# Performance work log

Hardware: AMD Instinct MI355X
Metric: run time of the kernel (lower is better)

The kernel has to match this reference:

```python
import jax, jax.numpy as jnp
import numpy as np

H = 16
D = 1024
Dh = D // H


def setup_inputs() -> dict:
    key = jax.random.key(0)
    ks = jax.random.split(key, 11)
    B, S = 2, 2048
    s = 1.0 / np.sqrt(D)
    inp = {
        'q': jax.random.normal(ks[0], (B, S, D), jnp.float32),
        'k': jax.random.normal(ks[1], (B, S, D), jnp.float32),
        'v': jax.random.normal(ks[2], (B, S, D), jnp.float32),
        'Wq': jax.random.normal(ks[3], (D, D), jnp.float32) * s,
        'bq': jnp.zeros((D,), jnp.float32),
        'Wk': jax.random.normal(ks[4], (D, D), jnp.float32) * s,
        'bk': jnp.zeros((D,), jnp.float32),
        'Wv': jax.random.normal(ks[5], (D, D), jnp.float32) * s,
        'bv': jnp.zeros((D,), jnp.float32),
        'Wo': jax.random.normal(ks[6], (D, D), jnp.float32) * s,
        'bo': jnp.zeros((D,), jnp.float32),
    }
    return inp


def reference(q, k, v, Wq, bq, Wk, bk, Wv, bv, Wo, bo):
    B, S, _ = q.shape
    # Linear projections (torch Linear: x @ W.T + b)
    qh = (q @ Wq.T + bq).reshape(B, S, H, Dh).transpose(0, 2, 1, 3)  # [B,H,S,Dh]
    kh = (k @ Wk.T + bk).reshape(B, S, H, Dh).transpose(0, 2, 1, 3)
    vh = (v @ Wv.T + bv).reshape(B, S, H, Dh).transpose(0, 2, 1, 3)
    # Scaled dot-product attention (mask=None, dropout=identity at eval)
    scores = jnp.einsum('bhqd,bhkd->bhqk', qh, kh) / jnp.sqrt(jnp.float32(Dh))
    a = jax.nn.softmax(scores, axis=-1)  # [B,H,S,S]
    o = jnp.einsum('bhqk,bhkd->bhqd', a, vh)
    o = o.transpose(0, 2, 1, 3).reshape(B, S, D)
    o = o @ Wo.T + bo
    return (o, a)
```

## Files before the change

kernel.cpp:

```cpp
#include <hip/hip_runtime.h>

typedef unsigned short u16;
typedef __bf16 bf16x8 __attribute__((ext_vector_type(8)));
typedef float f32x4 __attribute__((ext_vector_type(4)));

#define MFMA_BF16(a,b,c) __builtin_amdgcn_mfma_f32_16x16x32_bf16((a),(b),(c),0,0,0)

#define Bc 2
#define Sc 2048
#define Dc 1024
#define Hc 16
#define Dh 64
#define Mrows (Bc*Sc)

#define OFF_QB   0u
#define OFF_KB   4194304u
#define OFF_VB   8388608u
#define OFF_WQB  12582912u
#define OFF_WKB  13631488u
#define OFF_WVB  14680064u
#define OFF_WOB  15728640u
#define OFF_QP   16777216u
#define OFF_KP   20971520u
#define OFF_VP   25165824u
#define OFF_VT   29360128u
#define OFF_OH   33554432u

__device__ __forceinline__ u16 f32_to_bf16(float f) {
  unsigned u = __builtin_bit_cast(unsigned, f);
  u += 0x7FFFu + ((u >> 16) & 1u);
  return (u16)(u >> 16);
}
__device__ __forceinline__ float bf16_to_f32(u16 x) {
  return __builtin_bit_cast(float, ((unsigned)x) << 16);
}

__device__ __forceinline__ void gload16(const u16* g, u16* l) {
  __builtin_amdgcn_global_load_lds(
      (__attribute__((address_space(1))) void*)(g),
      (__attribute__((address_space(3))) void*)(l),
      16, 0, 0);
}

__global__ __launch_bounds__(256) void cvt_all(
    const float* __restrict__ q, const float* __restrict__ k, const float* __restrict__ v,
    const float* __restrict__ wq, const float* __restrict__ wk,
    const float* __restrict__ wv, const float* __restrict__ wo,
    u16* __restrict__ ws)
{
  int y = blockIdx.y;
  const float* src; u16* dst; int n;
  if (y < 3) {
    src = (y == 0) ? q : (y == 1) ? k : v;
    dst = ws + (unsigned)y * 4194304u;
    n = 4194304;
  } else {
    src = (y == 3) ? wq : (y == 4) ? wk : (y == 5) ? wv : wo;
    dst = ws + OFF_WQB + (unsigned)(y - 3) * 1048576u;
    n = 1048576;
  }
  int i = (blockIdx.x * 256 + threadIdx.x) * 8;
  if (i >= n) return;
  float4 f0 = *(const float4*)(src + i);
  float4 f1 = *(const float4*)(src + i + 4);
  u16 o[8];
  o[0] = f32_to_bf16(f0.x); o[1] = f32_to_bf16(f0.y);
  o[2] = f32_to_bf16(f0.z); o[3] = f32_to_bf16(f0.w);
  o[4] = f32_to_bf16(f1.x); o[5] = f32_to_bf16(f1.y);
  o[6] = f32_to_bf16(f1.z); o[7] = f32_to_bf16(f1.w);
  *(uint4*)(dst + i) = *(uint4*)o;
}

__device__ __forceinline__ void gemm128_body(
    const u16* __restrict__ X, const u16* __restrict__ W, const float* __restrict__ bias,
    u16* __restrict__ out_bf, float* __restrict__ out_f,
    u16* As, u16* Bs, int m0, int n0)
{
  int tid = threadIdx.x;
  int lane = tid & 63, w = tid >> 6;
  int wr = w >> 1, wc = w & 1;
  int qd = lane >> 4, ln = lane & 15;

  f32x4 acc[4][4];
#pragma unroll
  for (int i = 0; i < 4; i++)
#pragma unroll
    for (int j = 0; j < 4; j++) acc[i][j] = f32x4{0.f, 0.f, 0.f, 0.f};

  int srow = w * 16 + (lane >> 2);
  int scol = (lane & 3) * 8;
  const u16* Xa = X + (size_t)(m0 + srow) * 1024 + scol;
  const u16* Xb = Xa + (size_t)64 * 1024;
  const u16* Wa = W + (size_t)(n0 + srow) * 1024 + scol;
  const u16* Wb = Wa + (size_t)64 * 1024;
  u16* asA0 = As + (w * 16) * 32;
  u16* asA1 = As + (w * 16 + 64) * 32;
  u16* asB0 = Bs + (w * 16) * 32;
  u16* asB1 = Bs + (w * 16 + 64) * 32;

  for (int k0 = 0; k0 < 1024; k0 += 32) {
    __syncthreads();
    gload16(Xa + k0, asA0);
    gload16(Xb + k0, asA1);
    gload16(Wa + k0, asB0);
    gload16(Wb + k0, asB1);
    __syncthreads();
    bf16x8 af[4], bfr[4];
#pragma unroll
    for (int i = 0; i < 4; i++)
      af[i] = *(const bf16x8*)&As[(wr * 64 + i * 16 + ln) * 32 + qd * 8];
#pragma unroll
    for (int j = 0; j < 4; j++)
      bfr[j] = *(const bf16x8*)&Bs[(wc * 64 + j * 16 + ln) * 32 + qd * 8];
#pragma unroll
    for (int i = 0; i < 4; i++)
#pragma unroll
      for (int j = 0; j < 4; j++)
        acc[i][j] = MFMA_BF16(af[i], bfr[j], acc[i][j]);
  }

#pragma unroll
  for (int i = 0; i < 4; i++) {
#pragma unroll
    for (int j = 0; j < 4; j++) {
      int col = n0 + wc * 64 + j * 16 + ln;
      float bv = bias[col];
#pragma unroll
      for (int r = 0; r < 4; r++) {
        int row = m0 + wr * 64 + i * 16 + qd * 4 + r;
        float val = acc[i][j][r] + bv;
        if (out_bf) out_bf[(size_t)row * 1024 + col] = f32_to_bf16(val);
        else        out_f[(size_t)row * 1024 + col]  = val;
      }
    }
  }
}

__global__ __launch_bounds__(256) void qkv_gemm(
    const u16* __restrict__ xq, const u16* __restrict__ xk, const u16* __restrict__ xv,
    const u16* __restrict__ wq, const u16* __restrict__ wk, const u16* __restrict__ wv,
    const float* __restrict__ bq, const float* __restrict__ bk, const float* __restrict__ bv,
    u16* __restrict__ Qp, u16* __restrict__ Kp, u16* __restrict__ Vp)
{
  __shared__ __attribute__((aligned(16))) u16 As[128 * 32];
  __shared__ __attribute__((aligned(16))) u16 Bs[128 * 32];
  const u16 *X, *W; const float* bias; u16* out;
  int z = blockIdx.z;
  if (z == 0)      { X = xq; W = wq; bias = bq; out = Qp; }
  else if (z == 1) { X = xk; W = wk; bias = bk; out = Kp; }
  else             { X = xv; W = wv; bias = bv; out = Vp; }
  gemm128_body(X, W, bias, out, nullptr, As, Bs, blockIdx.y * 128, blockIdx.x * 128);
}

__global__ __launch_bounds__(256) void out_gemm(
    const u16* __restrict__ Oh, const u16* __restrict__ Wo, const float* __restrict__ bo,
    float* __restrict__ out)
{
  __shared__ __attribute__((aligned(16))) u16 As[128 * 32];
  __shared__ __attribute__((aligned(16))) u16 Bs[128 * 32];
  gemm128_body(Oh, Wo, bo, nullptr, out, As, Bs, blockIdx.y * 128, blockIdx.x * 128);
}

__global__ __launch_bounds__(256) void transpose_v(const u16* __restrict__ Vp, u16* __restrict__ Vt)
{
  __shared__ __attribute__((aligned(16))) u16 T[64 * 72];
  int tid = threadIdx.x;
  int st = blockIdx.x;
  int bh = blockIdx.y;
  int b = bh >> 4, h = bh & 15;
  int r0 = tid >> 3, c0 = (tid & 7) * 8;
  const u16* src = Vp + (size_t)(b * Sc + st * 64) * Dc + h * 64;
  *(uint4*)&T[r0 * 72 + c0]        = *(const uint4*)&src[(size_t)r0 * Dc + c0];
  *(uint4*)&T[(r0 + 32) * 72 + c0] = *(const uint4*)&src[(size_t)(r0 + 32) * Dc + c0];
  __syncthreads();
  u16* dst = Vt + (size_t)bh * 64 * Sc + st * 64;
  u16 tmp[8];
#pragma unroll
  for (int i = 0; i < 8; i++) tmp[i] = T[(c0 + i) * 72 + r0];
  *(uint4*)&dst[(size_t)r0 * Sc + c0] = *(uint4*)tmp;
#pragma unroll
  for (int i = 0; i < 8; i++) tmp[i] = T[(c0 + i) * 72 + r0 + 32];
  *(uint4*)&dst[(size_t)(r0 + 32) * Sc + c0] = *(uint4*)tmp;
}

#define BUFW (64 * 72)

__global__ __launch_bounds__(256) void attn_kernel(
    const u16* __restrict__ Qp, const u16* __restrict__ Kp, const u16* __restrict__ Vt,
    float* __restrict__ a_out, u16* __restrict__ Oh)
{
  __shared__ __attribute__((aligned(16))) u16 pool[5 * BUFW];
  __shared__ float Lb[4][64];
  u16* buf0 = pool;
  u16* buf1 = pool + BUFW;
  u16* buf2 = pool + 2 * BUFW;
  u16* buf3 = pool + 3 * BUFW;
  u16* Ps   = pool + 4 * BUFW;

  int tid = threadIdx.x;
  int lane = tid & 63, w = tid >> 6;
  int qd = lane >> 4, ln = lane & 15;
  int qb = blockIdx.x;
  int bh = blockIdx.y;
  int b = bh >> 4, h = bh & 15;

  const u16* Qg = Qp + (size_t)(b * Sc + qb * 64) * Dc + h * 64;
  const u16* Kg = Kp + (size_t)b * Sc * Dc + h * 64;
  const u16* Vg = Vt + (size_t)bh * 64 * Sc;

  int r0 = tid >> 3, c0 = (tid & 7) * 8;

  *(uint4*)&buf0[r0 * 72 + c0]        = *(const uint4*)&Qg[(size_t)r0 * Dc + c0];
  *(uint4*)&buf0[(r0 + 32) * 72 + c0] = *(const uint4*)&Qg[(size_t)(r0 + 32) * Dc + c0];
  *(uint4*)&buf1[r0 * 72 + c0]        = *(const uint4*)&Kg[(size_t)r0 * Dc + c0];
  *(uint4*)&buf1[(r0 + 32) * 72 + c0] = *(const uint4*)&Kg[(size_t)(r0 + 32) * Dc + c0];
  __syncthreads();

  bf16x8 af0[4], af1[4];
#pragma unroll
  for (int i = 0; i < 4; i++) {
    af0[i] = *(const bf16x8*)&buf0[(i * 16 + ln) * 72 + qd * 8];
    af1[i] = *(const bf16x8*)&buf0[(i * 16 + ln) * 72 + 32 + qd * 8];
  }
  bf16x8 qa0 = *(const bf16x8*)&buf0[(w * 16 + ln) * 72 + qd * 8];
  bf16x8 qa1 = *(const bf16x8*)&buf0[(w * 16 + ln) * 72 + 32 + qd * 8];

  const float cs = 0.125f * 1.44269504088896f;
  float l_acc[16];
#pragma unroll
  for (int t = 0; t < 16; t++) l_acc[t] = 0.f;

  for (int kt = 0; kt < 32; ++kt) {
    u16* cur = (kt & 1) ? buf2 : buf1;
    u16* nxt = (kt & 1) ? buf1 : buf2;
    uint4 ra, rb;
    if (kt < 31) {
      const u16* Kt_ = Kg + (size_t)((kt + 1) * 64) * Dc;
      ra = *(const uint4*)&Kt_[(size_t)r0 * Dc + c0];
      rb = *(const uint4*)&Kt_[(size_t)(r0 + 32) * Dc + c0];
    }
    bf16x8 b0 = *(const bf16x8*)&cur[(w * 16 + ln) * 72 + qd * 8];
    bf16x8 b1 = *(const bf16x8*)&cur[(w * 16 + ln) * 72 + 32 + qd * 8];
#pragma unroll
    for (int i = 0; i < 4; i++) {
      f32x4 s = f32x4{0.f, 0.f, 0.f, 0.f};
      s = MFMA_BF16(af0[i], b0, s);
      s = MFMA_BF16(af1[i], b1, s);
#pragma unroll
      for (int r = 0; r < 4; r++)
        l_acc[i * 4 + r] += exp2f(s[r] * cs);
    }
    if (kt < 31) {
      *(uint4*)&nxt[r0 * 72 + c0]        = ra;
      *(uint4*)&nxt[(r0 + 32) * 72 + c0] = rb;
    }
    __syncthreads();
  }

  uint4 ka0, ka1, va0, va1;
  {
    ka0 = *(const uint4*)&Kg[(size_t)r0 * Dc + c0];
    ka1 = *(const uint4*)&Kg[(size_t)(r0 + 32) * Dc + c0];
    va0 = *(const uint4*)&Vg[(size_t)r0 * Sc + c0];
    va1 = *(const uint4*)&Vg[(size_t)(r0 + 32) * Sc + c0];
  }

#pragma unroll
  for (int t = 0; t < 16; t++) {
    float v = l_acc[t];
    v += __shfl_xor(v, 1);
    v += __shfl_xor(v, 2);
    v += __shfl_xor(v, 4);
    v += __shfl_xor(v, 8);
    l_acc[t] = v;
  }
  if (ln == 0) {
#pragma unroll
    for (int i = 0; i < 4; i++)
#pragma unroll
      for (int r = 0; r < 4; r++)
        Lb[w][i * 16 + qd * 4 + r] = l_acc[i * 4 + r];
  }
  *(uint4*)&buf1[r0 * 72 + c0]        = ka0;
  *(uint4*)&buf1[(r0 + 32) * 72 + c0] = ka1;
  *(uint4*)&buf0[r0 * 72 + c0]        = va0;
  *(uint4*)&buf0[(r0 + 32) * 72 + c0] = va1;
  __syncthreads();

  float inv_l[4];
#pragma unroll
  for (int r = 0; r < 4; r++) {
    int row = w * 16 + qd * 4 + r;
    inv_l[r] = 1.f / (Lb[0][row] + Lb[1][row] + Lb[2][row] + Lb[3][row]);
  }

  f32x4 o[4];
#pragma unroll
  for (int j = 0; j < 4; j++) o[j] = f32x4{0.f, 0.f, 0.f, 0.f};
  float* a_base = a_out + ((size_t)bh * Sc + qb * 64) * Sc;
  u16* Pw = Ps + w * 16 * 72;

  for (int kt = 0; kt < 32; ++kt) {
    u16* Kcur = (kt & 1) ? buf2 : buf1;
    u16* Knxt = (kt & 1) ? buf1 : buf2;
    u16* Vcur = (kt & 1) ? buf3 : buf0;
    u16* Vnxt = (kt & 1) ? buf0 : buf3;
    uint4 ra0, ra1, rv0, rv1;
    if (kt < 31) {
      const u16* Kt_ = Kg + (size_t)((kt + 1) * 64) * Dc;
      const u16* Vt_ = Vg + (kt + 1) * 64;
      ra0 = *(const uint4*)&Kt_[(size_t)r0 * Dc + c0];
      ra1 = *(const uint4*)&Kt_[(size_t)(r0 + 32) * Dc + c0];
      rv0 = *(const uint4*)&Vt_[(size_t)r0 * Sc + c0];
      rv1 = *(const uint4*)&Vt_[(size_t)(r0 + 32) * Sc + c0];
    }
    f32x4 s[4];
#pragma unroll
    for (int j = 0; j < 4; j++) {
      s[j] = f32x4{0.f, 0.f, 0.f, 0.f};
      bf16x8 b0 = *(const bf16x8*)&Kcur[(j * 16 + ln) * 72 + qd * 8];
      bf16x8 b1 = *(const bf16x8*)&Kcur[(j * 16 + ln) * 72 + 32 + qd * 8];
      s[j] = MFMA_BF16(qa0, b0, s[j]);
      s[j] = MFMA_BF16(qa1, b1, s[j]);
    }
#pragma unroll
    for (int j = 0; j < 4; j++) {
#pragma unroll
      for (int r = 0; r < 4; r++) {
        float p = exp2f(s[j][r] * cs) * inv_l[r];
        Pw[(qd * 4 + r) * 72 + j * 16 + ln] = f32_to_bf16(p);
      }
    }
    bf16x8 pa0 = *(const bf16x8*)&Pw[ln * 72 + qd * 8];
    bf16x8 pa1 = *(const bf16x8*)&Pw[ln * 72 + 32 + qd * 8];
#pragma unroll
    for (int j = 0; j < 4; j++) {
      bf16x8 vb0 = *(const bf16x8*)&Vcur[(j * 16 + ln) * 72 + qd * 8];
      bf16x8 vb1 = *(const bf16x8*)&Vcur[(j * 16 + ln) * 72 + 32 + qd * 8];
      o[j] = MFMA_BF16(pa0, vb0, o[j]);
      o[j] = MFMA_BF16(pa1, vb1, o[j]);
    }
#pragma unroll
    for (int t = 0; t < 4; t++) {
      int chunk = lane + 64 * t;
      int row = chunk >> 4;
      int colc = (chunk & 15) * 4;
      u16 p4[4];
      *(uint2*)p4 = *(const uint2*)&Pw[row * 72 + colc];
      float4 f;
      f.x = bf16_to_f32(p4[0]); f.y = bf16_to_f32(p4[1]);
      f.z = bf16_to_f32(p4[2]); f.w = bf16_to_f32(p4[3]);
      *(float4*)&a_base[(size_t)(w * 16 + row) * Sc + kt * 64 + colc] = f;
    }
    if (kt < 31) {
      *(uint4*)&Knxt[r0 * 72 + c0]        = ra0;
      *(uint4*)&Knxt[(r0 + 32) * 72 + c0] = ra1;
      *(uint4*)&Vnxt[r0 * 72 + c0]        = rv0;
      *(uint4*)&Vnxt[(r0 + 32) * 72 + c0] = rv1;
    }
    __syncthreads();
  }

  u16* Og = Oh + (size_t)(b * Sc + qb * 64) * Dc + h * 64;
#pragma unroll
  for (int j = 0; j < 4; j++)
#pragma unroll
    for (int r = 0; r < 4; r++)
      Og[(size_t)(w * 16 + qd * 4 + r) * Dc + j * 16 + ln] = f32_to_bf16(o[j][r]);
}

extern "C" void kernel_launch(void* const* d_in, const int* in_sizes, int n_in,
                              void* d_out, int out_size, void* d_ws, size_t ws_size,
                              hipStream_t stream)
{
  const float* q  = (const float*)d_in[0];
  const float* k  = (const float*)d_in[1];
  const float* v  = (const float*)d_in[2];
  const float* Wq = (const float*)d_in[3];
  const float* bq = (const float*)d_in[4];
  const float* Wk = (const float*)d_in[5];
  const float* bk = (const float*)d_in[6];
  const float* Wv = (const float*)d_in[7];
  const float* bv = (const float*)d_in[8];
  const float* Wo = (const float*)d_in[9];
  const float* bo = (const float*)d_in[10];

  u16* ws = (u16*)d_ws;
  u16* qb  = ws + OFF_QB;
  u16* kb  = ws + OFF_KB;
  u16* vb  = ws + OFF_VB;
  u16* Wqb = ws + OFF_WQB;
  u16* Wkb = ws + OFF_WKB;
  u16* Wvb = ws + OFF_WVB;
  u16* Wob = ws + OFF_WOB;
  u16* Qp  = ws + OFF_QP;
  u16* Kp  = ws + OFF_KP;
  u16* Vp  = ws + OFF_VP;
  u16* Vt  = ws + OFF_VT;
  u16* Oh  = ws + OFF_OH;

  float* out_o = (float*)d_out;
  float* out_a = out_o + 4194304;

  cvt_all<<<dim3(2048, 7), 256, 0, stream>>>(q, k, v, Wq, Wk, Wv, Wo, ws);
  qkv_gemm<<<dim3(8, 32, 3), 256, 0, stream>>>(qb, kb, vb, Wqb, Wkb, Wvb, bq, bk, bv, Qp, Kp, Vp);
  transpose_v<<<dim3(32, 32), 256, 0, stream>>>(Vp, Vt);
  attn_kernel<<<dim3(32, 32), 256, 0, stream>>>(Qp, Kp, Vt, out_a, Oh);
  out_gemm<<<dim3(8, 32), 256, 0, stream>>>(Oh, Wob, bo, out_o);
}
```

Baseline: 765.1 us.

## Split attention into row-sum and PV kernels with XCD-aware block swizzle

```diff
diff --git a/kernel.cpp b/kernel.cpp
--- a/kernel.cpp
+++ b/kernel.cpp
@@ -42,6 +42,14 @@
       16, 0, 0);
 }
 
+__device__ __forceinline__ void swz_qb_bh(int* qb, int* bh) {
+  int flat = blockIdx.y * 32 + blockIdx.x;
+  int xcd = flat & 7;
+  int idx = flat >> 3;
+  *bh = xcd * 4 + (idx >> 5);
+  *qb = idx & 31;
+}
+
 __global__ __launch_bounds__(256) void cvt_all(
     const float* __restrict__ q, const float* __restrict__ k, const float* __restrict__ v,
     const float* __restrict__ wq, const float* __restrict__ wk,
@@ -183,47 +191,31 @@
   *(uint4*)&dst[(size_t)(r0 + 32) * Sc + c0] = *(uint4*)tmp;
 }
 
-#define BUFW (64 * 72)
-
-__global__ __launch_bounds__(256) void attn_kernel(
-    const u16* __restrict__ Qp, const u16* __restrict__ Kp, const u16* __restrict__ Vt,
-    float* __restrict__ a_out, u16* __restrict__ Oh)
-{
-  __shared__ __attribute__((aligned(16))) u16 pool[5 * BUFW];
+__global__ __launch_bounds__(256) void attn_lsum(
+    const u16* __restrict__ Qp, const u16* __restrict__ Kp, float* __restrict__ l_out)
+{
+  __shared__ __attribute__((aligned(16))) u16 Qs[64 * 72];
+  __shared__ __attribute__((aligned(16))) u16 Kb0[64 * 72];
+  __shared__ __attribute__((aligned(16))) u16 Kb1[64 * 72];
   __shared__ float Lb[4][64];
-  u16* buf0 = pool;
-  u16* buf1 = pool + BUFW;
-  u16* buf2 = pool + 2 * BUFW;
-  u16* buf3 = pool + 3 * BUFW;
-  u16* Ps   = pool + 4 * BUFW;
 
   int tid = threadIdx.x;
   int lane = tid & 63, w = tid >> 6;
   int qd = lane >> 4, ln = lane & 15;
-  int qb = blockIdx.x;
-  int bh = blockIdx.y;
+  int qb, bh;
+  swz_qb_bh(&qb, &bh);
   int b = bh >> 4, h = bh & 15;
 
   const u16* Qg = Qp + (size_t)(b * Sc + qb * 64) * Dc + h * 64;
   const u16* Kg = Kp + (size_t)b * Sc * Dc + h * 64;
-  const u16* Vg = Vt + (size_t)bh * 64 * Sc;
 
   int r0 = tid >> 3, c0 = (tid & 7) * 8;
 
-  *(uint4*)&buf0[r0 * 72 + c0]        = *(const uint4*)&Qg[(size_t)r0 * Dc + c0];
-  *(uint4*)&buf0[(r0 + 32) * 72 + c0] = *(const uint4*)&Qg[(size_t)(r0 + 32) * Dc + c0];
-  *(uint4*)&buf1[r0 * 72 + c0]        = *(const uint4*)&Kg[(size_t)r0 * Dc + c0];
-  *(uint4*)&buf1[(r0 + 32) * 72 + c0] = *(const uint4*)&Kg[(size_t)(r0 + 32) * Dc + c0];
+  *(uint4*)&Qs[r0 * 72 + c0]         = *(const uint4*)&Qg[(size_t)r0 * Dc + c0];
+  *(uint4*)&Qs[(r0 + 32) * 72 + c0]  = *(const uint4*)&Qg[(size_t)(r0 + 32) * Dc + c0];
+  *(uint4*)&Kb0[r0 * 72 + c0]        = *(const uint4*)&Kg[(size_t)r0 * Dc + c0];
+  *(uint4*)&Kb0[(r0 + 32) * 72 + c0] = *(const uint4*)&Kg[(size_t)(r0 + 32) * Dc + c0];
   __syncthreads();
-
-  bf16x8 af0[4], af1[4];
-#pragma unroll
-  for (int i = 0; i < 4; i++) {
-    af0[i] = *(const bf16x8*)&buf0[(i * 16 + ln) * 72 + qd * 8];
-    af1[i] = *(const bf16x8*)&buf0[(i * 16 + ln) * 72 + 32 + qd * 8];
-  }
-  bf16x8 qa0 = *(const bf16x8*)&buf0[(w * 16 + ln) * 72 + qd * 8];
-  bf16x8 qa1 = *(const bf16x8*)&buf0[(w * 16 + ln) * 72 + 32 + qd * 8];
 
   const float cs = 0.125f * 1.44269504088896f;
   float l_acc[16];
@@ -231,8 +223,8 @@
   for (int t = 0; t < 16; t++) l_acc[t] = 0.f;
 
   for (int kt = 0; kt < 32; ++kt) {
-    u16* cur = (kt & 1) ? buf2 : buf1;
-    u16* nxt = (kt & 1) ? buf1 : buf2;
+    u16* cur = (kt & 1) ? Kb1 : Kb0;
+    u16* nxt = (kt & 1) ? Kb0 : Kb1;
     uint4 ra, rb;
     if (kt < 31) {
       const u16* Kt_ = Kg + (size_t)((kt + 1) * 64) * Dc;
@@ -243,9 +235,11 @@
     bf16x8 b1 = *(const bf16x8*)&cur[(w * 16 + ln) * 72 + 32 + qd * 8];
 #pragma unroll
     for (int i = 0; i < 4; i++) {
+      bf16x8 af0 = *(const bf16x8*)&Qs[(i * 16 + ln) * 72 + qd * 8];
+      bf16x8 af1 = *(const bf16x8*)&Qs[(i * 16 + ln) * 72 + 32 + qd * 8];
       f32x4 s = f32x4{0.f, 0.f, 0.f, 0.f};
-      s = MFMA_BF16(af0[i], b0, s);
-      s = MFMA_BF16(af1[i], b1, s);
+      s = MFMA_BF16(af0, b0, s);
+      s = MFMA_BF16(af1, b1, s);
 #pragma unroll
       for (int r = 0; r < 4; r++)
         l_acc[i * 4 + r] += exp2f(s[r] * cs);
@@ -255,14 +249,6 @@
       *(uint4*)&nxt[(r0 + 32) * 72 + c0] = rb;
     }
     __syncthreads();
-  }
-
-  uint4 ka0, ka1, va0, va1;
-  {
-    ka0 = *(const uint4*)&Kg[(size_t)r0 * Dc + c0];
-    ka1 = *(const uint4*)&Kg[(size_t)(r0 + 32) * Dc + c0];
-    va0 = *(const uint4*)&Vg[(size_t)r0 * Sc + c0];
-    va1 = *(const uint4*)&Vg[(size_t)(r0 + 32) * Sc + c0];
   }
 
 #pragma unroll
@@ -281,19 +267,54 @@
       for (int r = 0; r < 4; r++)
         Lb[w][i * 16 + qd * 4 + r] = l_acc[i * 4 + r];
   }
-  *(uint4*)&buf1[r0 * 72 + c0]        = ka0;
-  *(uint4*)&buf1[(r0 + 32) * 72 + c0] = ka1;
-  *(uint4*)&buf0[r0 * 72 + c0]        = va0;
-  *(uint4*)&buf0[(r0 + 32) * 72 + c0] = va1;
   __syncthreads();
+  if (tid < 64) {
+    float lsum = Lb[0][tid] + Lb[1][tid] + Lb[2][tid] + Lb[3][tid];
+    l_out[(size_t)bh * Sc + qb * 64 + tid] = lsum;
+  }
+}
+
+#define BUFW (64 * 72)
+
+__global__ __launch_bounds__(256) void attn_pv(
+    const u16* __restrict__ Qp, const u16* __restrict__ Kp, const u16* __restrict__ Vt,
+    const float* __restrict__ l_in, float* __restrict__ a_out, u16* __restrict__ Oh)
+{
+  __shared__ __attribute__((aligned(16))) u16 pool[5 * BUFW];
+  u16* buf0 = pool;
+  u16* buf1 = pool + BUFW;
+  u16* buf2 = pool + 2 * BUFW;
+  u16* buf3 = pool + 3 * BUFW;
+  u16* Ps   = pool + 4 * BUFW;
+
+  int tid = threadIdx.x;
+  int lane = tid & 63, w = tid >> 6;
+  int qd = lane >> 4, ln = lane & 15;
+  int qb, bh;
+  swz_qb_bh(&qb, &bh);
+  int b = bh >> 4, h = bh & 15;
+
+  const u16* Qg = Qp + (size_t)(b * Sc + qb * 64) * Dc + h * 64;
+  const u16* Kg = Kp + (size_t)b * Sc * Dc + h * 64;
+  const u16* Vg = Vt + (size_t)bh * 64 * Sc;
+
+  int r0 = tid >> 3, c0 = (tid & 7) * 8;
+
+  bf16x8 qa0 = *(const bf16x8*)&Qg[(size_t)(w * 16 + ln) * Dc + qd * 8];
+  bf16x8 qa1 = *(const bf16x8*)&Qg[(size_t)(w * 16 + ln) * Dc + 32 + qd * 8];
 
   float inv_l[4];
 #pragma unroll
-  for (int r = 0; r < 4; r++) {
-    int row = w * 16 + qd * 4 + r;
-    inv_l[r] = 1.f / (Lb[0][row] + Lb[1][row] + Lb[2][row] + Lb[3][row]);
-  }
-
+  for (int r = 0; r < 4; r++)
+    inv_l[r] = 1.f / l_in[(size_t)bh * Sc + qb * 64 + w * 16 + qd * 4 + r];
+
+  *(uint4*)&buf0[r0 * 72 + c0]        = *(const uint4*)&Kg[(size_t)r0 * Dc + c0];
+  *(uint4*)&buf0[(r0 + 32) * 72 + c0] = *(const uint4*)&Kg[(size_t)(r0 + 32) * Dc + c0];
+  *(uint4*)&buf2[r0 * 72 + c0]        = *(const uint4*)&Vg[(size_t)r0 * Sc + c0];
+  *(uint4*)&buf2[(r0 + 32) * 72 + c0] = *(const uint4*)&Vg[(size_t)(r0 + 32) * Sc + c0];
+  __syncthreads();
+
+  const float cs = 0.125f * 1.44269504088896f;
   f32x4 o[4];
 #pragma unroll
   for (int j = 0; j < 4; j++) o[j] = f32x4{0.f, 0.f, 0.f, 0.f};
@@ -301,10 +322,10 @@
   u16* Pw = Ps + w * 16 * 72;
 
   for (int kt = 0; kt < 32; ++kt) {
-    u16* Kcur = (kt & 1) ? buf2 : buf1;
-    u16* Knxt = (kt & 1) ? buf1 : buf2;
-    u16* Vcur = (kt & 1) ? buf3 : buf0;
-    u16* Vnxt = (kt & 1) ? buf0 : buf3;
+    u16* Kcur = (kt & 1) ? buf1 : buf0;
+    u16* Knxt = (kt & 1) ? buf0 : buf1;
+    u16* Vcur = (kt & 1) ? buf3 : buf2;
+    u16* Vnxt = (kt & 1) ? buf2 : buf3;
     uint4 ra0, ra1, rv0, rv1;
     if (kt < 31) {
       const u16* Kt_ = Kg + (size_t)((kt + 1) * 64) * Dc;
@@ -330,15 +351,6 @@
         float p = exp2f(s[j][r] * cs) * inv_l[r];
         Pw[(qd * 4 + r) * 72 + j * 16 + ln] = f32_to_bf16(p);
       }
-    }
-    bf16x8 pa0 = *(const bf16x8*)&Pw[ln * 72 + qd * 8];
-    bf16x8 pa1 = *(const bf16x8*)&Pw[ln * 72 + 32 + qd * 8];
-#pragma unroll
-    for (int j = 0; j < 4; j++) {
-      bf16x8 vb0 = *(const bf16x8*)&Vcur[(j * 16 + ln) * 72 + qd * 8];
-      bf16x8 vb1 = *(const bf16x8*)&Vcur[(j * 16 + ln) * 72 + 32 + qd * 8];
-      o[j] = MFMA_BF16(pa0, vb0, o[j]);
-      o[j] = MFMA_BF16(pa1, vb1, o[j]);
     }
 #pragma unroll
     for (int t = 0; t < 4; t++) {
@@ -351,6 +363,15 @@
       f.x = bf16_to_f32(p4[0]); f.y = bf16_to_f32(p4[1]);
       f.z = bf16_to_f32(p4[2]); f.w = bf16_to_f32(p4[3]);
       *(float4*)&a_base[(size_t)(w * 16 + row) * Sc + kt * 64 + colc] = f;
+    }
+    bf16x8 pa0 = *(const bf16x8*)&Pw[ln * 72 + qd * 8];
+    bf16x8 pa1 = *(const bf16x8*)&Pw[ln * 72 + 32 + qd * 8];
+#pragma unroll
+    for (int j = 0; j < 4; j++) {
+      bf16x8 vb0 = *(const bf16x8*)&Vcur[(j * 16 + ln) * 72 + qd * 8];
+      bf16x8 vb1 = *(const bf16x8*)&Vcur[(j * 16 + ln) * 72 + 32 + qd * 8];
+      o[j] = MFMA_BF16(pa0, vb0, o[j]);
+      o[j] = MFMA_BF16(pa1, vb1, o[j]);
     }
     if (kt < 31) {
       *(uint4*)&Knxt[r0 * 72 + c0]        = ra0;
@@ -398,6 +419,7 @@
   u16* Vp  = ws + OFF_VP;
   u16* Vt  = ws + OFF_VT;
   u16* Oh  = ws + OFF_OH;
+  float* lbuf = (float*)(ws + OFF_QB);
 
   float* out_o = (float*)d_out;
   float* out_a = out_o + 4194304;
@@ -405,6 +427,7 @@
   cvt_all<<<dim3(2048, 7), 256, 0, stream>>>(q, k, v, Wq, Wk, Wv, Wo, ws);
   qkv_gemm<<<dim3(8, 32, 3), 256, 0, stream>>>(qb, kb, vb, Wqb, Wkb, Wvb, bq, bk, bv, Qp, Kp, Vp);
   transpose_v<<<dim3(32, 32), 256, 0, stream>>>(Vp, Vt);
-  attn_kernel<<<dim3(32, 32), 256, 0, stream>>>(Qp, Kp, Vt, out_a, Oh);
+  attn_lsum<<<dim3(32, 32), 256, 0, stream>>>(Qp, Kp, lbuf);
+  attn_pv<<<dim3(32, 32), 256, 0, stream>>>(Qp, Kp, Vt, lbuf, out_a, Oh);
   out_gemm<<<dim3(8, 32), 256, 0, stream>>>(Oh, Wob, bo, out_o);
 }
```

Result: no change. 768.3 us (+0.4%).
